# Performance work log

Hardware: AMD Instinct MI355X
Metric: run time of the kernel (lower is better)

## Reference

```python
import jax, jax.numpy as jnp
import numpy as np

B, C, L, MID, HID, OUT, K = 4096, 6, 1024, 512, 512, 256, 5
EPS = 1e-5


def _bn_eval(x, g, b, m, v):
    # BatchNorm1d eval mode on (B, C, T): normalize per channel with running stats
    inv = g / jnp.sqrt(v + EPS)
    return (x - m[None, :, None]) * inv[None, :, None] + b[None, :, None]


def setup_inputs() -> dict:
    key = jax.random.key(0)
    ks = jax.random.split(key, 12)
    s_in = 1.0 / np.sqrt(L)
    s_hid = 1.0 / np.sqrt(HID)
    inp = {
        "x": jax.random.normal(ks[0], (B, C, L), jnp.float32),
        # k stacked self-attention branches (two Linear(L, MID) each)
        "aW1": jax.random.normal(ks[1], (K, L, MID), jnp.float32) * s_in,
        "ab1": jnp.zeros((K, MID), jnp.float32),
        "aW2": jax.random.normal(ks[2], (K, L, MID), jnp.float32) * s_in,
        "ab2": jnp.zeros((K, MID), jnp.float32),
        # linearExchangeLayer: Linear(K*C, C)
        "linW": jax.random.normal(ks[3], (K * C, C), jnp.float32) / np.sqrt(K * C),
        "linb": jnp.zeros((C,), jnp.float32),
        # GraphConvolution weights
        "gW1": jax.random.normal(ks[4], (L, HID), jnp.float32) * s_in,
        "gb1": jnp.zeros((HID,), jnp.float32),
        "gW2": jax.random.normal(ks[5], (HID, OUT), jnp.float32) * s_hid,
        "gb2": jnp.zeros((OUT,), jnp.float32),
        # PReLU (single shared parameter, torch default 0.25)
        "prelu_a": jnp.array(0.25, jnp.float32),
        # BatchNorm1d params + running stats (eval mode)
        "bn1_g": jnp.ones((C,), jnp.float32),
        "bn1_b": jnp.zeros((C,), jnp.float32),
        "bn1_m": jnp.zeros((C,), jnp.float32),
        "bn1_v": jnp.ones((C,), jnp.float32),
        "bn2_g": jnp.ones((C,), jnp.float32),
        "bn2_b": jnp.zeros((C,), jnp.float32),
        "bn2_m": jnp.zeros((C,), jnp.float32),
        "bn2_v": jnp.ones((C,), jnp.float32),
    }
    return inp


def reference(x, aW1, ab1, aW2, ab2, linW, linb, gW1, gb1, gW2, gb2,
              prelu_a, bn1_g, bn1_b, bn1_m, bn1_v, bn2_g, bn2_b, bn2_m, bn2_v):
    b, c, l = x.shape
    k = aW1.shape[0]
    # --- multi-head attention adjacency: (b, c, c) ---
    q = jnp.einsum('bcl,klm->bkcm', x, aW1) + ab1[None, :, None, :]
    kv = jnp.einsum('bcl,klm->bkcm', x, aW2) + ab2[None, :, None, :]
    scores = jax.nn.softmax(jnp.einsum('bkcm,bkdm->bkcd', q, kv), axis=-1)
    # concat heads along last dim: (b, c, k*c)
    cat = scores.transpose(0, 2, 1, 3).reshape(b, c, k * c)
    A = jax.nn.softmax(cat @ linW + linb, axis=-1)  # (b, c, c)
    # --- GraphConvolution 1 (dropout identity in eval) ---
    h = jnp.einsum('bcd,bdh->bch', A, x @ gW1) + gb1
    # PReLU then BatchNorm1d
    h = jnp.where(h >= 0, h, prelu_a * h)
    h = _bn_eval(h, bn1_g, bn1_b, bn1_m, bn1_v)
    # --- GraphConvolution 2 ---
    out = jnp.einsum('bcd,bdh->bch', A, h @ gW2) + gb2
    out = _bn_eval(out, bn2_g, bn2_b, bn2_m, bn2_v)
    return out
```

## Files before the change

kernel.cpp:

```cpp
#include <hip/hip_runtime.h>
#include <hip/hip_bf16.h>


using bf16 = __hip_bfloat16;
using s16x8 = __attribute__((ext_vector_type(8))) short;
using f32x4 = __attribute__((ext_vector_type(4))) float;

#define AS1(p) ((__attribute__((address_space(1))) void*)((void*)(p)))
#define AS3(p) ((__attribute__((address_space(3))) void*)(p))

#if defined(__has_builtin)
#if __has_builtin(__builtin_amdgcn_global_load_lds)
#define HAVE_GLL 1
#endif
#endif

__device__ __forceinline__ float s2f(short s) {
  union { unsigned int u; float f; } c;
  c.u = ((unsigned int)(unsigned short)s) << 16;
  return c.f;
}
__device__ __forceinline__ short f2s(float x) {
  bf16 b = __float2bfloat16(x);
  short s;
  __builtin_memcpy(&s, &b, 2);
  return s;
}

struct GJob {
  const bf16* Bt;
  const float* bias;
  int boff;
  bf16* out;
};
struct ScJob {
  const bf16* Q;
  const bf16* KV;
  float* S;
  int head;
};

__global__ __launch_bounds__(256) void prep_kernel(
    const float* __restrict__ x, bf16* __restrict__ Xb, int do_cvt,
    const float* __restrict__ aW1, bf16* __restrict__ W1T,
    const float* __restrict__ aW2, bf16* __restrict__ W2T,
    const float* __restrict__ gW1, bf16* __restrict__ G1T,
    const float* __restrict__ gW2, bf16* __restrict__ G2T) {
  const int bid = blockIdx.x, tid = threadIdx.x;
  if (bid < 12288) {
    if (!do_cvt) return;
    int i = bid * 256 + tid;
    float4 p0 = ((const float4*)x)[i * 2];
    float4 p1 = ((const float4*)x)[i * 2 + 1];
    s16x8 v;
    v[0] = f2s(p0.x); v[1] = f2s(p0.y); v[2] = f2s(p0.z); v[3] = f2s(p0.w);
    v[4] = f2s(p1.x); v[5] = f2s(p1.y); v[6] = f2s(p1.z); v[7] = f2s(p1.w);
    ((s16x8*)Xb)[i] = v;
    return;
  }
  int r = bid - 12288;
  const float* src; short* dst; int R, C, bx, by;
  if (r < 2560) {
    int z = r >> 9, q = r & 511;
    src = aW1 + (size_t)z * 524288; dst = (short*)W1T + (size_t)z * 524288;
    R = 1024; C = 512; bx = q & 31; by = q >> 5;
  } else if (r < 5120) {
    r -= 2560;
    int z = r >> 9, q = r & 511;
    src = aW2 + (size_t)z * 524288; dst = (short*)W2T + (size_t)z * 524288;
    R = 1024; C = 512; bx = q & 31; by = q >> 5;
  } else if (r < 5632) {
    r -= 5120;
    src = gW1; dst = (short*)G1T; R = 1024; C = 512; bx = r & 31; by = r >> 5;
  } else {
    r -= 5632;
    src = gW2; dst = (short*)G2T; R = 512; C = 256; bx = r & 15; by = r >> 4;
  }
  __shared__ short tile[32][33];
  const int tx = tid & 31, ty = tid >> 5;
  const int r0 = bx * 32, c0 = by * 32;
#pragma unroll
  for (int i = 0; i < 4; ++i)
    tile[ty + i * 8][tx] = f2s(src[(size_t)(r0 + ty + i * 8) * C + c0 + tx]);
  __syncthreads();
#pragma unroll
  for (int i = 0; i < 4; ++i)
    dst[(size_t)(c0 + ty + i * 8) * R + r0 + tx] = tile[tx][ty + i * 8];
}

__device__ __forceinline__ void scores_wave(
    const bf16* __restrict__ Q, const bf16* __restrict__ KV,
    float* __restrict__ S, int head, int b0, int lane) {
  const int l16 = lane & 15, quad = lane >> 4;
  const int lr0 = (l16 < 8) ? l16 : (l16 - 8);
  const int lr = (lr0 <= 5) ? lr0 : 5;
  const int gb = (l16 < 8) ? b0 : (b0 + 1);
  const int gr = gb * 6 + lr;

  const short* qrow = (const short*)Q + (size_t)gr * 512 + quad * 8;
  const short* krow = (const short*)KV + (size_t)gr * 512 + quad * 8;

  f32x4 acc = (f32x4){0.f, 0.f, 0.f, 0.f};
#pragma unroll
  for (int kk = 0; kk < 16; ++kk) {
    s16x8 a = *(const s16x8*)(qrow + kk * 32);
    s16x8 b = *(const s16x8*)(krow + kk * 32);
    acc = __builtin_amdgcn_mfma_f32_16x16x32_bf16(a, b, acc, 0, 0, 0);
  }

  if (l16 < 6) {
#pragma unroll
    for (int r = 0; r < 4; ++r) {
      int m = quad * 4 + r;
      if (m < 6)
        S[((size_t)b0 * 5 + head) * 36 + m * 6 + l16] = acc[r];
    }
  } else if (l16 >= 8 && l16 < 14) {
#pragma unroll
    for (int r = 0; r < 4; ++r) {
      int m = quad * 4 + r;
      if (m >= 8 && m < 14)
        S[((size_t)(b0 + 1) * 5 + head) * 36 + (m - 8) * 6 + (l16 - 8)] = acc[r];
    }
  }
}

__global__ __launch_bounds__(256) void scores_mfma2(
    const bf16* __restrict__ Q0, const bf16* __restrict__ KV0,
    const bf16* __restrict__ Q1, const bf16* __restrict__ KV1,
    float* __restrict__ S, int head0) {
  const int h = blockIdx.y;
  const int lane = threadIdx.x & 63, w = threadIdx.x >> 6;
  const int b0 = (blockIdx.x * 4 + w) * 2;
  scores_wave(h ? Q1 : Q0, h ? KV1 : KV0, S, head0 + h, b0, lane);
}

template <int AF32>
__global__ __launch_bounds__(256) void gemm_bt(
    const void* __restrict__ Ag,
    const bf16* __restrict__ Bt0, const bf16* __restrict__ Bt1,
    const float* __restrict__ bias0, const float* __restrict__ bias1, int boff,
    bf16* __restrict__ out0, bf16* __restrict__ out1,
    int M, int N, int K) {
  const bf16* Bt = (blockIdx.z == 0) ? Bt0 : Bt1;
  const float* bias = (blockIdx.z == 0) ? bias0 : bias1;
  bf16* Cg = (blockIdx.z == 0) ? out0 : out1;

  __shared__ short lA[128 * 32];
  __shared__ short lB[128 * 32];

  const int tid = threadIdx.x;
  const int lane = tid & 63, w = tid >> 6;
  const int wr = w >> 1, wc = w & 1;
  const int l16 = lane & 15, quad = lane >> 4;
  const int lrow = lane >> 2;
  const int scol = (((lane & 3) ^ ((lane >> 3) & 3)) * 8);

  const size_t rm0 = (size_t)blockIdx.x * 128;
  const size_t cn0 = (size_t)blockIdx.y * 128;

  f32x4 acc[4][4];
#pragma unroll
  for (int i = 0; i < 4; ++i)
#pragma unroll
    for (int j = 0; j < 4; ++j) acc[i][j] = (f32x4){0.f, 0.f, 0.f, 0.f};

  for (int kb = 0; kb < K; kb += 32) {
#pragma unroll
    for (int t = 0; t < 2; ++t) {
      int chunk = w * 2 + t;
      int row = chunk * 16 + lrow;
      const bf16* gb = Bt + (cn0 + row) * (size_t)K + kb + scol;
#ifdef HAVE_GLL
      __builtin_amdgcn_global_load_lds(AS1(gb), AS3(lB + chunk * 512), 16, 0, 0);
#else
      *(s16x8*)(lB + chunk * 512 + lane * 8) = *(const s16x8*)gb;
#endif
      if (AF32) {
        const float* ga = (const float*)Ag + (rm0 + row) * (size_t)K + kb + scol;
        float4 p0 = *(const float4*)ga;
        float4 p1 = *(const float4*)(ga + 4);
        s16x8 v;
        v[0] = f2s(p0.x); v[1] = f2s(p0.y); v[2] = f2s(p0.z); v[3] = f2s(p0.w);
        v[4] = f2s(p1.x); v[5] = f2s(p1.y); v[6] = f2s(p1.z); v[7] = f2s(p1.w);
        *(s16x8*)(lA + chunk * 512 + lane * 8) = v;
      } else {
        const bf16* ga = (const bf16*)Ag + (rm0 + row) * (size_t)K + kb + scol;
#ifdef HAVE_GLL
        __builtin_amdgcn_global_load_lds(AS1(ga), AS3(lA + chunk * 512), 16, 0, 0);
#else
        *(s16x8*)(lA + chunk * 512 + lane * 8) = *(const s16x8*)ga;
#endif
      }
    }
    __syncthreads();

    const int q2 = (quad ^ ((l16 >> 1) & 3)) * 8;
    s16x8 af[4], bfv[4];
#pragma unroll
    for (int i = 0; i < 4; ++i) {
      af[i] = *(const s16x8*)(lA + (wr * 64 + i * 16 + l16) * 32 + q2);
      bfv[i] = *(const s16x8*)(lB + (wc * 64 + i * 16 + l16) * 32 + q2);
    }
#pragma unroll
    for (int i = 0; i < 4; ++i)
#pragma unroll
      for (int j = 0; j < 4; ++j)
        acc[i][j] = __builtin_amdgcn_mfma_f32_16x16x32_bf16(af[i], bfv[j], acc[i][j], 0, 0, 0);
    __syncthreads();
  }

#pragma unroll
  for (int j = 0; j < 4; ++j) {
    size_t col = cn0 + wc * 64 + j * 16 + l16;
    float bv = bias ? bias[boff + col] : 0.f;
#pragma unroll
    for (int i = 0; i < 4; ++i) {
      size_t rowb = rm0 + wr * 64 + i * 16 + quad * 4;
#pragma unroll
      for (int r = 0; r < 4; ++r) {
        float v = acc[i][j][r] + bv;
        Cg[(rowb + r) * (size_t)N + col] = __float2bfloat16(v);
      }
    }
  }
}

__global__ __launch_bounds__(512, 2) void gemm256_8ph(
    const bf16* __restrict__ A,
    GJob j0, GJob j1, GJob j2, GJob j3,
    int nzg, ScJob s0, ScJob s1,
    int M, int N, int K) {
  if ((int)blockIdx.z >= nzg) {
    ScJob sc = ((int)blockIdx.z == nzg) ? s0 : s1;
    const int lane = threadIdx.x & 63, w = threadIdx.x >> 6;
    const int stride = gridDim.x * gridDim.y * 8;
    const int base = ((int)blockIdx.y * gridDim.x + blockIdx.x) * 8 + w;
    for (int job = base; job < 2048; job += stride)
      scores_wave(sc.Q, sc.KV, sc.S, sc.head, job * 2, lane);
    return;
  }

  const GJob j = (blockIdx.z == 0) ? j0 : (blockIdx.z == 1) ? j1
               : (blockIdx.z == 2) ? j2 : j3;
  const bf16* Bt = j.Bt;
  const float* bias = j.bias;
  const int boff = j.boff;
  bf16* Cg = j.out;

  __shared__ __attribute__((aligned(16))) short ldsS[65536];

  const int tid = threadIdx.x;
  const int w = tid >> 6, l = tid & 63;
  const int l16 = l & 15, quad = l >> 4;
  const int wr = w >> 2, wc = w & 3;

  const size_t rm0 = (size_t)blockIdx.x * 256;
  const size_t cn0 = (size_t)blockIdx.y * 256;

  const int colS = ((l & 7) ^ (l >> 3)) * 8;
  const int rowS = w * 16 + (l >> 3);
  const short* pAs = (const short*)A + (rm0 + rowS) * (size_t)K + colS;
  const short* pBs = (const short*)Bt + (cn0 + rowS) * (size_t)K + colS;

  const int u0 = (quad ^ (l16 & 7)) * 8;
  const int u1 = ((quad + 4) ^ (l16 & 7)) * 8;

  f32x4 acc[8][4];
#pragma unroll
  for (int i = 0; i < 8; ++i)
#pragma unroll
    for (int j2i = 0; j2i < 4; ++j2i) acc[i][j2i] = (f32x4){0.f, 0.f, 0.f, 0.f};

  s16x8 af[4][2], bf0[2][2], bf1[2][2];

  const int T = K >> 6;

#ifdef HAVE_GLL
#define SA(BUF, H, KB) do {                                                          \
    __builtin_amdgcn_global_load_lds(AS1(pAs + (size_t)((H) * 128) * K + (KB)),      \
        AS3(ldsS + (BUF) * 32768 + (H) * 8192 + w * 1024), 16, 0, 0);                \
    __builtin_amdgcn_global_load_lds(AS1(pAs + (size_t)((H) * 128 + 8) * K + (KB)),  \
        AS3(ldsS + (BUF) * 32768 + (H) * 8192 + w * 1024 + 512), 16, 0, 0);          \
  } while (0)
#define SB(BUF, H, KB) do {                                                          \
    __builtin_amdgcn_global_load_lds(AS1(pBs + (size_t)((H) * 128) * K + (KB)),      \
        AS3(ldsS + (BUF) * 32768 + 16384 + (H) * 8192 + w * 1024), 16, 0, 0);        \
    __builtin_amdgcn_global_load_lds(AS1(pBs + (size_t)((H) * 128 + 8) * K + (KB)),  \
        AS3(ldsS + (BUF) * 32768 + 16384 + (H) * 8192 + w * 1024 + 512), 16, 0, 0);  \
  } while (0)
#else
#define SA(BUF, H, KB) do {                                                          \
    *(s16x8*)(ldsS + (BUF) * 32768 + (H) * 8192 + w * 1024 + l * 8) =                \
        *(const s16x8*)(pAs + (size_t)((H) * 128) * K + (KB));                       \
    *(s16x8*)(ldsS + (BUF) * 32768 + (H) * 8192 + w * 1024 + 512 + l * 8) =          \
        *(const s16x8*)(pAs + (size_t)((H) * 128 + 8) * K + (KB));                   \
  } while (0)
#define SB(BUF, H, KB) do {                                                          \
    *(s16x8*)(ldsS + (BUF) * 32768 + 16384 + (H) * 8192 + w * 1024 + l * 8) =        \
        *(const s16x8*)(pBs + (size_t)((H) * 128) * K + (KB));                       \
    *(s16x8*)(ldsS + (BUF) * 32768 + 16384 + (H) * 8192 + w * 1024 + 512 + l * 8) =  \
        *(const s16x8*)(pBs + (size_t)((H) * 128 + 8) * K + (KB));                   \
  } while (0)
#endif

#define LDA(BUF, MH) do {                                                            \
    _Pragma("unroll") for (int i = 0; i < 4; ++i) {                                  \
      const short* bse = ldsS + (BUF) * 32768 + wr * 8192 + (MH) * 4096 +            \
                         i * 1024 + l16 * 64;                                        \
      af[i][0] = *(const s16x8*)(bse + u0);                                          \
      af[i][1] = *(const s16x8*)(bse + u1);                                          \
    }                                                                                \
  } while (0)

#define LDB(BUF, NH, DST) do {                                                       \
    _Pragma("unroll") for (int n = 0; n < 2; ++n) {                                  \
      const short* bse = ldsS + (BUF) * 32768 + 16384 + (wc >> 1) * 8192 +           \
                         (wc & 1) * 4096 + (NH) * 2048 + n * 1024 + l16 * 64;        \
      DST[n][0] = *(const s16x8*)(bse + u0);                                         \
      DST[n][1] = *(const s16x8*)(bse + u1);                                         \
    }                                                                                \
  } while (0)

#define MFMAQ(MH, NH, BSET) do {                                                     \
    _Pragma("unroll") for (int i = 0; i < 4; ++i)                                    \
      _Pragma("unroll") for (int n = 0; n < 2; ++n) {                                \
        acc[(MH) * 4 + i][(NH) * 2 + n] = __builtin_amdgcn_mfma_f32_16x16x32_bf16(   \
            af[i][0], BSET[n][0], acc[(MH) * 4 + i][(NH) * 2 + n], 0, 0, 0);         \
        acc[(MH) * 4 + i][(NH) * 2 + n] = __builtin_amdgcn_mfma_f32_16x16x32_bf16(   \
            af[i][1], BSET[n][1], acc[(MH) * 4 + i][(NH) * 2 + n], 0, 0, 0);         \
      }                                                                              \
  } while (0)

#define BARX() asm volatile("s_barrier" ::: "memory")
#define LGKM0() do { asm volatile("s_waitcnt lgkmcnt(0)" ::: "memory");              \
                     __builtin_amdgcn_sched_barrier(0); } while (0)
#define VM6() do { asm volatile("s_waitcnt vmcnt(6)" ::: "memory");                  \
                   __builtin_amdgcn_sched_barrier(0); } while (0)

#define TILE_STEP(BUF, t) do {                                                       \
    const int kN_ = ((t) + 1 < T ? (t) + 1 : T - 1) << 6;                            \
    const int k2_ = ((t) + 2 < T ? (t) + 2 : T - 1) << 6;                            \
               \
    LDA(BUF, 0); LDB(BUF, 0, bf0); LDB(BUF, 1, bf1);                                 \
    SA((BUF) ^ 1, 1, kN_);                                                           \
    BARX(); LGKM0();                                                                 \
    __builtin_amdgcn_s_setprio(1); MFMAQ(0, 0, bf0); __builtin_amdgcn_s_setprio(0);  \
    BARX();                                                                          \
                        \
    SB(BUF, 0, k2_);                                                                 \
    BARX();                                                                          \
    __builtin_amdgcn_s_setprio(1); MFMAQ(0, 1, bf1); __builtin_amdgcn_s_setprio(0);  \
    BARX();                                                                          \
                                               \
    LDA(BUF, 1);                                                                     \
    SB(BUF, 1, k2_);                                                                 \
    BARX(); LGKM0();                                                                 \
    __builtin_amdgcn_s_setprio(1); MFMAQ(1, 1, bf1); __builtin_amdgcn_s_setprio(0);  \
    BARX();                                                                          \
                         \
    SA(BUF, 0, k2_);                                                                 \
    VM6();                                                                           \
    BARX();                                                                          \
    __builtin_amdgcn_s_setprio(1); MFMAQ(1, 0, bf0); __builtin_amdgcn_s_setprio(0);  \
    BARX();                                                                          \
  } while (0)

  {
    const int k1_ = (T > 1 ? 1 : 0) << 6;
    SB(0, 0, 0); SB(0, 1, 0); SA(0, 0, 0); SA(0, 1, 0);
    SB(1, 0, k1_); SB(1, 1, k1_); SA(1, 0, k1_);
    VM6();
    BARX();
  }

  for (int t = 0; t < T; t += 2) {
    TILE_STEP(0, t);
    TILE_STEP(1, t + 1);
  }

#pragma unroll
  for (int jj = 0; jj < 4; ++jj) {
    size_t col = cn0 + wc * 64 + jj * 16 + l16;
    float bv = bias ? bias[boff + col] : 0.f;
#pragma unroll
    for (int i = 0; i < 8; ++i) {
      size_t rowb = rm0 + wr * 128 + i * 16 + quad * 4;
#pragma unroll
      for (int r = 0; r < 4; ++r) {
        Cg[(rowb + r) * (size_t)N + col] = __float2bfloat16(acc[i][jj][r] + bv);
      }
    }
  }
#undef SA
#undef SB
#undef LDA
#undef LDB
#undef MFMAQ
#undef BARX
#undef LGKM0
#undef VM6
#undef TILE_STEP
}

__global__ __launch_bounds__(256) void batch_mid4(
    const float* __restrict__ S, const bf16* __restrict__ XG,
    const bf16* __restrict__ Q4, const bf16* __restrict__ KV4, int fuse5,
    const float* __restrict__ linW, const float* __restrict__ linb,
    const float* __restrict__ gb1, const float* __restrict__ prelu,
    const float* __restrict__ g1, const float* __restrict__ b1,
    const float* __restrict__ m1, const float* __restrict__ v1,
    float* __restrict__ Afull, bf16* __restrict__ H) {
  const int tid = threadIdx.x, g = tid >> 6, t = tid & 63;
  const int b = blockIdx.x * 4 + g;
  __shared__ float p[4][5][6][6];
  __shared__ float Ar[4][6][6];
  __shared__ float lw[30][6];
  __shared__ float lbv[6], sc1[6], sm1[6], sb1[6];

  if (tid < 30) {
#pragma unroll
    for (int j = 0; j < 6; ++j) lw[tid][j] = linW[tid * 6 + j];
  }
  if (tid < 6) {
    lbv[tid] = linb[tid];
    sc1[tid] = g1[tid] * rsqrtf(v1[tid] + 1e-5f);
    sm1[tid] = m1[tid];
    sb1[tid] = b1[tid];
  }
  if (fuse5 && t < 36) {
    int c = t / 6, d = t % 6;
    const s16x8* qr = (const s16x8*)((const short*)Q4 + ((size_t)b * 6 + c) * 512);
    const s16x8* kr = (const s16x8*)((const short*)KV4 + ((size_t)b * 6 + d) * 512);
    float acc = 0.f;
#pragma unroll 4
    for (int i = 0; i < 64; ++i) {
      s16x8 qa = qr[i], kb = kr[i];
#pragma unroll
      for (int j = 0; j < 8; ++j) acc += s2f(qa[j]) * s2f(kb[j]);
    }
    p[g][4][c][d] = acc;
  }
  __syncthreads();

  if (t < 30) {
    int k = t / 6, c = t % 6;
    float v[6];
    if (k == 4 && fuse5) {
#pragma unroll
      for (int d = 0; d < 6; ++d) v[d] = p[g][4][c][d];
    } else {
      const float* sp = S + ((size_t)b * 5 + k) * 36 + c * 6;
#pragma unroll
      for (int d = 0; d < 6; ++d) v[d] = sp[d];
    }
    float mx = v[0];
#pragma unroll
    for (int d = 1; d < 6; ++d) mx = fmaxf(mx, v[d]);
    float s = 0.f;
#pragma unroll
    for (int d = 0; d < 6; ++d) { v[d] = expf(v[d] - mx); s += v[d]; }
    float inv = 1.f / s;
#pragma unroll
    for (int d = 0; d < 6; ++d) p[g][k][c][d] = v[d] * inv;
  }
  __syncthreads();

  if (t < 6) {
    int c = t;
    float ap[6];
#pragma unroll
    for (int j = 0; j < 6; ++j) ap[j] = lbv[j];
    for (int k = 0; k < 5; ++k)
#pragma unroll
      for (int d = 0; d < 6; ++d) {
        float pv = p[g][k][c][d];
#pragma unroll
        for (int j = 0; j < 6; ++j) ap[j] += pv * lw[k * 6 + d][j];
      }
    float mx = ap[0];
#pragma unroll
    for (int j = 1; j < 6; ++j) mx = fmaxf(mx, ap[j]);
    float s = 0.f;
#pragma unroll
    for (int j = 0; j < 6; ++j) { ap[j] = expf(ap[j] - mx); s += ap[j]; }
    float inv = 1.f / s;
#pragma unroll
    for (int j = 0; j < 6; ++j) {
      float a = ap[j] * inv;
      Ar[g][c][j] = a;
      Afull[(size_t)b * 36 + c * 6 + j] = a;
    }
  }
  __syncthreads();

  float pa = prelu[0];
  for (int col = t; col < 512; col += 64) {
    float xg[6];
#pragma unroll
    for (int d = 0; d < 6; ++d) xg[d] = s2f(((const short*)XG)[((size_t)b * 6 + d) * 512 + col]);
    float gbv = gb1[col];
#pragma unroll
    for (int c = 0; c < 6; ++c) {
      float h = gbv;
#pragma unroll
      for (int d = 0; d < 6; ++d) h += Ar[g][c][d] * xg[d];
      h = (h >= 0.f) ? h : pa * h;
      h = (h - sm1[c]) * sc1[c] + sb1[c];
      H[((size_t)b * 6 + c) * 512 + col] = __float2bfloat16(h);
    }
  }
}

__global__ __launch_bounds__(256) void batch_out4(
    const float* __restrict__ Afull, const bf16* __restrict__ HW,
    const float* __restrict__ gb2,
    const float* __restrict__ g2, const float* __restrict__ b2,
    const float* __restrict__ m2, const float* __restrict__ v2,
    float* __restrict__ out) {
  const int tid = threadIdx.x, g = tid >> 6, t = tid & 63;
  const int b = blockIdx.x * 4 + g;
  __shared__ float Ar[4][36];
  __shared__ float sc[6], sm[6], sb[6];
  if (t < 36) Ar[g][t] = Afull[(size_t)b * 36 + t];
  if (tid < 6) {
    sc[tid] = g2[tid] * rsqrtf(v2[tid] + 1e-5f);
    sm[tid] = m2[tid];
    sb[tid] = b2[tid];
  }
  __syncthreads();
  for (int col = t; col < 256; col += 64) {
    float hw[6];
#pragma unroll
    for (int d = 0; d < 6; ++d) hw[d] = s2f(((const short*)HW)[((size_t)b * 6 + d) * 256 + col]);
    float gv = gb2[col];
#pragma unroll
    for (int c = 0; c < 6; ++c) {
      float o = gv;
#pragma unroll
      for (int d = 0; d < 6; ++d) o += Ar[g][c * 6 + d] * hw[d];
      o = (o - sm[c]) * sc[c] + sb[c];
      out[((size_t)b * 6 + c) * 256 + col] = o;
    }
  }
}

extern "C" void kernel_launch(void* const* d_in, const int* in_sizes, int n_in,
                              void* d_out, int out_size, void* d_ws, size_t ws_size,
                              hipStream_t stream) {
  const float* x    = (const float*)d_in[0];
  const float* aW1  = (const float*)d_in[1];
  const float* ab1  = (const float*)d_in[2];
  const float* aW2  = (const float*)d_in[3];
  const float* ab2  = (const float*)d_in[4];
  const float* linW = (const float*)d_in[5];
  const float* linb = (const float*)d_in[6];
  const float* gW1  = (const float*)d_in[7];
  const float* gb1  = (const float*)d_in[8];
  const float* gW2  = (const float*)d_in[9];
  const float* gb2  = (const float*)d_in[10];
  const float* prelu = (const float*)d_in[11];
  const float* bn1g = (const float*)d_in[12];
  const float* bn1b = (const float*)d_in[13];
  const float* bn1m = (const float*)d_in[14];
  const float* bn1v = (const float*)d_in[15];
  const float* bn2g = (const float*)d_in[16];
  const float* bn2b = (const float*)d_in[17];
  const float* bn2m = (const float*)d_in[18];
  const float* bn2v = (const float*)d_in[19];

  char* ws = (char*)d_ws;
  bf16* W1T   = (bf16*)(ws + 0);
  bf16* W2T   = (bf16*)(ws + 5242880);
  bf16* G1T   = (bf16*)(ws + 10485760);
  bf16* G2T   = (bf16*)(ws + 11534336);
  float* S    = (float*)(ws + 11796480);
  float* Af   = (float*)(ws + 14745600);
  bf16* BufA  = (bf16*)(ws + 15335424);
  bf16* BufB  = (bf16*)(ws + 40501248);
  bf16* Xb    = (bf16*)(ws + 65667072);
  bf16* BufA2 = (bf16*)(ws + 115998720);
  bf16* BufB2 = (bf16*)(ws + 141164544);
  bf16* BufA3 = (bf16*)(ws + 166330368);
  bf16* BufB3 = (bf16*)(ws + 191496192);
  bf16* BufA4 = (bf16*)(ws + 216662016);
  bf16* BufB4 = (bf16*)(ws + 241827840);
  const bool big  = ws_size >= 115998720ull;
  const bool big2 = ws_size >= 166330368ull;
  const bool big3 = ws_size >= 266993664ull;

  prep_kernel<<<18048, 256, 0, stream>>>(x, Xb, big ? 1 : 0,
                                         aW1, W1T, aW2, W2T, gW1, G1T, gW2, G2T);

  ScJob scz{nullptr, nullptr, nullptr, 0};

  if (big3) {
    GJob q0{W1T, ab1, 0, BufA},                 k0{W2T, ab2, 0, BufB};
    GJob q1{W1T + 524288, ab1, 512, BufA2},     k1{W2T + 524288, ab2, 512, BufB2};
    gemm256_8ph<<<dim3(96, 2, 4), 512, 0, stream>>>(
        Xb, q0, k0, q1, k1, 4, scz, scz, 24576, 512, 1024);
    GJob q2{W1T + 2 * 524288, ab1, 1024, BufA3}, k2{W2T + 2 * 524288, ab2, 1024, BufB3};
    GJob q3{W1T + 3 * 524288, ab1, 1536, BufA4}, k3{W2T + 3 * 524288, ab2, 1536, BufB4};
    ScJob sA{BufA, BufB, S, 0}, sB{BufA2, BufB2, S, 1};
    gemm256_8ph<<<dim3(96, 2, 6), 512, 0, stream>>>(
        Xb, q2, k2, q3, k3, 4, sA, sB, 24576, 512, 1024);
    GJob q4{W1T + 4 * 524288, ab1, 2048, BufA}, k4{W2T + 4 * 524288, ab2, 2048, BufB};
    GJob jxg{G1T, nullptr, 0, BufA2};
    ScJob sC{BufA3, BufB3, S, 2}, sD{BufA4, BufB4, S, 3};
    gemm256_8ph<<<dim3(96, 2, 5), 512, 0, stream>>>(
        Xb, q4, k4, jxg, jxg, 3, sC, sD, 24576, 512, 1024);
    batch_mid4<<<1024, 256, 0, stream>>>(S, BufA2, BufA, BufB, 1, linW, linb,
                                         gb1, prelu, bn1g, bn1b, bn1m, bn1v,
                                         Af, BufB2);
  } else if (big2) {
    for (int k = 0; k < 4; k += 2) {
      GJob qa{W1T + (size_t)k * 524288, ab1, k * 512, BufA};
      GJob ka{W2T + (size_t)k * 524288, ab2, k * 512, BufB};
      GJob qb{W1T + (size_t)(k + 1) * 524288, ab1, (k + 1) * 512, BufA2};
      GJob kb{W2T + (size_t)(k + 1) * 524288, ab2, (k + 1) * 512, BufB2};
      gemm256_8ph<<<dim3(96, 2, 4), 512, 0, stream>>>(
          Xb, qa, ka, qb, kb, 4, scz, scz, 24576, 512, 1024);
      scores_mfma2<<<dim3(512, 2), 256, 0, stream>>>(BufA, BufB, BufA2, BufB2, S, k);
    }
    GJob q4{W1T + 4 * 524288, ab1, 2048, BufA}, k4{W2T + 4 * 524288, ab2, 2048, BufB};
    GJob jxg{G1T, nullptr, 0, BufA2};
    gemm256_8ph<<<dim3(96, 2, 3), 512, 0, stream>>>(
        Xb, q4, k4, jxg, jxg, 4, scz, scz, 24576, 512, 1024);
    batch_mid4<<<1024, 256, 0, stream>>>(S, BufA2, BufA, BufB, 1, linW, linb,
                                         gb1, prelu, bn1g, bn1b, bn1m, bn1v,
                                         Af, BufB2);
  } else if (big) {
    for (int k = 0; k < 5; ++k) {
      GJob q{W1T + (size_t)k * 524288, ab1, k * 512, BufA};
      GJob kk{W2T + (size_t)k * 524288, ab2, k * 512, BufB};
      gemm256_8ph<<<dim3(96, 2, 2), 512, 0, stream>>>(
          Xb, q, kk, q, kk, 4, scz, scz, 24576, 512, 1024);
      scores_mfma2<<<dim3(512, 1), 256, 0, stream>>>(BufA, BufB, BufA, BufB, S, k);
    }
    GJob jxg{G1T, nullptr, 0, BufA};
    gemm256_8ph<<<dim3(96, 2, 1), 512, 0, stream>>>(
        Xb, jxg, jxg, jxg, jxg, 4, scz, scz, 24576, 512, 1024);
    batch_mid4<<<1024, 256, 0, stream>>>(S, BufA, BufA, BufA, 0, linW, linb,
                                         gb1, prelu, bn1g, bn1b, bn1m, bn1v,
                                         Af, BufB);
  } else {
    for (int k = 0; k < 5; ++k) {
      const bf16* w1 = W1T + (size_t)k * 524288;
      const bf16* w2 = W2T + (size_t)k * 524288;
      gemm_bt<1><<<dim3(192, 4, 2), 256, 0, stream>>>(
          x, w1, w2, ab1, ab2, k * 512, BufA, BufB, 24576, 512, 1024);
      scores_mfma2<<<dim3(512, 1), 256, 0, stream>>>(BufA, BufB, BufA, BufB, S, k);
    }
    gemm_bt<1><<<dim3(192, 4, 1), 256, 0, stream>>>(
        x, G1T, G1T, nullptr, nullptr, 0, BufA, BufA, 24576, 512, 1024);
    batch_mid4<<<1024, 256, 0, stream>>>(S, BufA, BufA, BufA, 0, linW, linb,
                                         gb1, prelu, bn1g, bn1b, bn1m, bn1v,
                                         Af, BufB);
  }

  bf16* Hbuf = big2 ? BufB2 : BufB;
  gemm_bt<0><<<dim3(192, 2, 1), 256, 0, stream>>>(
      Hbuf, G2T, G2T, nullptr, nullptr, 0, BufA, BufA, 24576, 256, 512);

  batch_out4<<<1024, 256, 0, stream>>>(Af, BufA, gb2, bn2g, bn2b, bn2m, bn2v,
                                       (float*)d_out);
}
```

Before: 636.6 us.

## Reassociate graph conv as (A·X)·W1, batch all projection GEMMs in one launch

Result: no change. 629.9 us (-1.1%).

```diff
diff --git a/kernel.cpp b/kernel.cpp
--- a/kernel.cpp
+++ b/kernel.cpp
@@ -33,22 +33,18 @@
   int boff;
   bf16* out;
 };
-struct ScJob {
-  const bf16* Q;
-  const bf16* KV;
-  float* S;
-  int head;
+struct GJobs10 {
+  GJob j[10];
 };
 
 __global__ __launch_bounds__(256) void prep_kernel(
-    const float* __restrict__ x, bf16* __restrict__ Xb, int do_cvt,
+    const float* __restrict__ x, bf16* __restrict__ Xb,
     const float* __restrict__ aW1, bf16* __restrict__ W1T,
     const float* __restrict__ aW2, bf16* __restrict__ W2T,
     const float* __restrict__ gW1, bf16* __restrict__ G1T,
     const float* __restrict__ gW2, bf16* __restrict__ G2T) {
   const int bid = blockIdx.x, tid = threadIdx.x;
   if (bid < 12288) {
-    if (!do_cvt) return;
     int i = bid * 256 + tid;
     float4 p0 = ((const float4*)x)[i * 2];
     float4 p1 = ((const float4*)x)[i * 2 + 1];
@@ -88,17 +84,17 @@
     dst[(size_t)(c0 + ty + i * 8) * R + r0 + tx] = tile[tx][ty + i * 8];
 }
 
-__device__ __forceinline__ void scores_wave(
-    const bf16* __restrict__ Q, const bf16* __restrict__ KV,
-    float* __restrict__ S, int head, int b0, int lane) {
+__device__ __forceinline__ void scores_grp(
+    const bf16* __restrict__ Qa, const bf16* __restrict__ Ka,
+    const bf16* __restrict__ Qb, const bf16* __restrict__ Kb,
+    int rowA, int rowB,
+    float* __restrict__ dstA, float* __restrict__ dstB,
+    int lane) {
   const int l16 = lane & 15, quad = lane >> 4;
-  const int lr0 = (l16 < 8) ? l16 : (l16 - 8);
-  const int lr = (lr0 <= 5) ? lr0 : 5;
-  const int gb = (l16 < 8) ? b0 : (b0 + 1);
-  const int gr = gb * 6 + lr;
-
-  const short* qrow = (const short*)Q + (size_t)gr * 512 + quad * 8;
-  const short* krow = (const short*)KV + (size_t)gr * 512 + quad * 8;
+  int lr = l16 & 7; if (lr > 5) lr = 5;
+  const int gr = ((l16 < 8) ? rowA : rowB) + lr;
+  const short* qrow = (const short*)((l16 < 8) ? Qa : Qb) + (size_t)gr * 512 + quad * 8;
+  const short* krow = (const short*)((l16 < 8) ? Ka : Kb) + (size_t)gr * 512 + quad * 8;
 
   f32x4 acc = (f32x4){0.f, 0.f, 0.f, 0.f};
 #pragma unroll
@@ -112,15 +108,13 @@
 #pragma unroll
     for (int r = 0; r < 4; ++r) {
       int m = quad * 4 + r;
-      if (m < 6)
-        S[((size_t)b0 * 5 + head) * 36 + m * 6 + l16] = acc[r];
+      if (m < 6) dstA[m * 6 + l16] = acc[r];
     }
   } else if (l16 >= 8 && l16 < 14) {
 #pragma unroll
     for (int r = 0; r < 4; ++r) {
       int m = quad * 4 + r;
-      if (m >= 8 && m < 14)
-        S[((size_t)(b0 + 1) * 5 + head) * 36 + (m - 8) * 6 + (l16 - 8)] = acc[r];
+      if (m >= 8 && m < 14) dstB[(m - 8) * 6 + (l16 - 8)] = acc[r];
     }
   }
 }
@@ -130,9 +124,14 @@
     const bf16* __restrict__ Q1, const bf16* __restrict__ KV1,
     float* __restrict__ S, int head0) {
   const int h = blockIdx.y;
+  const bf16* Q = h ? Q1 : Q0;
+  const bf16* KV = h ? KV1 : KV0;
+  const int head = head0 + h;
   const int lane = threadIdx.x & 63, w = threadIdx.x >> 6;
   const int b0 = (blockIdx.x * 4 + w) * 2;
-  scores_wave(h ? Q1 : Q0, h ? KV1 : KV0, S, head0 + h, b0, lane);
+  scores_grp(Q, KV, Q, KV, b0 * 6, (b0 + 1) * 6,
+             S + ((size_t)b0 * 5 + head) * 36,
+             S + ((size_t)(b0 + 1) * 5 + head) * 36, lane);
 }
 
 template <int AF32>
@@ -227,33 +226,31 @@
 }
 
 __global__ __launch_bounds__(512, 2) void gemm256_8ph(
-    const bf16* __restrict__ A,
-    GJob j0, GJob j1, GJob j2, GJob j3,
-    int nzg, ScJob s0, ScJob s1,
+    const bf16* __restrict__ A, GJobs10 jobs, int epi_z,
+    const float* __restrict__ prelu_p,
+    const float* __restrict__ bn_g, const float* __restrict__ bn_b,
+    const float* __restrict__ bn_m, const float* __restrict__ bn_v,
     int M, int N, int K) {
-  if ((int)blockIdx.z >= nzg) {
-    ScJob sc = ((int)blockIdx.z == nzg) ? s0 : s1;
-    const int lane = threadIdx.x & 63, w = threadIdx.x >> 6;
-    const int stride = gridDim.x * gridDim.y * 8;
-    const int base = ((int)blockIdx.y * gridDim.x + blockIdx.x) * 8 + w;
-    for (int job = base; job < 2048; job += stride)
-      scores_wave(sc.Q, sc.KV, sc.S, sc.head, job * 2, lane);
-    return;
-  }
-
-  const GJob j = (blockIdx.z == 0) ? j0 : (blockIdx.z == 1) ? j1
-               : (blockIdx.z == 2) ? j2 : j3;
-  const bf16* Bt = j.Bt;
-  const float* bias = j.bias;
-  const int boff = j.boff;
-  bf16* Cg = j.out;
+  const GJob jb = jobs.j[blockIdx.z];
+  const bf16* Bt = jb.Bt;
+  const float* bias = jb.bias;
+  const int boff = jb.boff;
+  bf16* Cg = jb.out;
+  const bool EPI = (epi_z == (int)blockIdx.z);
 
   __shared__ __attribute__((aligned(16))) short ldsS[65536];
+  __shared__ float epi_s[12];
 
   const int tid = threadIdx.x;
   const int w = tid >> 6, l = tid & 63;
   const int l16 = l & 15, quad = l >> 4;
   const int wr = w >> 2, wc = w & 3;
+
+  if (EPI && tid < 6) {
+    float s = bn_g[tid] * rsqrtf(bn_v[tid] + 1e-5f);
+    epi_s[tid] = s;
+    epi_s[6 + tid] = bn_b[tid] - bn_m[tid] * s;
+  }
 
   const size_t rm0 = (size_t)blockIdx.x * 256;
   const size_t cn0 = (size_t)blockIdx.y * 256;
@@ -379,18 +376,35 @@
     TILE_STEP(1, t + 1);
   }
 
+  float pa = EPI ? prelu_p[0] : 0.f;
+  short* st = ldsS + w * 8192;
 #pragma unroll
   for (int jj = 0; jj < 4; ++jj) {
-    size_t col = cn0 + wc * 64 + jj * 16 + l16;
-    float bv = bias ? bias[boff + col] : 0.f;
+    int coll = jj * 16 + l16;
+    float bv = bias ? bias[boff + (int)cn0 + wc * 64 + coll] : 0.f;
 #pragma unroll
     for (int i = 0; i < 8; ++i) {
-      size_t rowb = rm0 + wr * 128 + i * 16 + quad * 4;
 #pragma unroll
       for (int r = 0; r < 4; ++r) {
-        Cg[(rowb + r) * (size_t)N + col] = __float2bfloat16(acc[i][jj][r] + bv);
+        int rowl = i * 16 + quad * 4 + r;
+        float v = acc[i][jj][r] + bv;
+        if (EPI) {
+          v = (v >= 0.f) ? v : pa * v;
+          int c = (int)((rm0 + wr * 128 + rowl) % 6);
+          v = v * epi_s[c] + epi_s[6 + c];
+        }
+        st[rowl * 64 + coll] = f2s(v);
       }
     }
+  }
+  __syncthreads();
+#pragma unroll
+  for (int it = 0; it < 16; ++it) {
+    int rowl = it * 8 + (l >> 3);
+    int cch = (l & 7) * 8;
+    s16x8 vv = *(const s16x8*)(st + rowl * 64 + cch);
+    *(s16x8*)((short*)Cg + (rm0 + wr * 128 + rowl) * (size_t)N +
+              cn0 + wc * 64 + cch) = vv;
   }
 #undef SA
 #undef SB
@@ -403,57 +417,50 @@
 #undef TILE_STEP
 }
 
-__global__ __launch_bounds__(256) void batch_mid4(
-    const float* __restrict__ S, const bf16* __restrict__ XG,
-    const bf16* __restrict__ Q4, const bf16* __restrict__ KV4, int fuse5,
+template <int ALLP>
+__global__ __launch_bounds__(256) void mid5(
+    const float* __restrict__ S,
+    const bf16* __restrict__ Q0, const bf16* __restrict__ Q1,
+    const bf16* __restrict__ Q2, const bf16* __restrict__ Q3,
+    const bf16* __restrict__ K0, const bf16* __restrict__ K1,
+    const bf16* __restrict__ K2, const bf16* __restrict__ K3,
+    const bf16* __restrict__ Q4, const bf16* __restrict__ K4,
+    bf16* __restrict__ Xb,
     const float* __restrict__ linW, const float* __restrict__ linb,
-    const float* __restrict__ gb1, const float* __restrict__ prelu,
-    const float* __restrict__ g1, const float* __restrict__ b1,
-    const float* __restrict__ m1, const float* __restrict__ v1,
-    float* __restrict__ Afull, bf16* __restrict__ H) {
+    float* __restrict__ Afull) {
   const int tid = threadIdx.x, g = tid >> 6, t = tid & 63;
   const int b = blockIdx.x * 4 + g;
   __shared__ float p[4][5][6][6];
   __shared__ float Ar[4][6][6];
   __shared__ float lw[30][6];
-  __shared__ float lbv[6], sc1[6], sm1[6], sb1[6];
+  __shared__ float lbv[6];
 
   if (tid < 30) {
 #pragma unroll
     for (int j = 0; j < 6; ++j) lw[tid][j] = linW[tid * 6 + j];
   }
-  if (tid < 6) {
-    lbv[tid] = linb[tid];
-    sc1[tid] = g1[tid] * rsqrtf(v1[tid] + 1e-5f);
-    sm1[tid] = m1[tid];
-    sb1[tid] = b1[tid];
-  }
-  if (fuse5 && t < 36) {
-    int c = t / 6, d = t % 6;
-    const s16x8* qr = (const s16x8*)((const short*)Q4 + ((size_t)b * 6 + c) * 512);
-    const s16x8* kr = (const s16x8*)((const short*)KV4 + ((size_t)b * 6 + d) * 512);
-    float acc = 0.f;
-#pragma unroll 4
-    for (int i = 0; i < 64; ++i) {
-      s16x8 qa = qr[i], kb = kr[i];
-#pragma unroll
-      for (int j = 0; j < 8; ++j) acc += s2f(qa[j]) * s2f(kb[j]);
-    }
-    p[g][4][c][d] = acc;
+  if (tid < 6) lbv[tid] = linb[tid];
+
+  const int r6 = b * 6;
+  if (ALLP) {
+    scores_grp(Q0, K0, Q1, K1, r6, r6, &p[g][0][0][0], &p[g][1][0][0], t);
+    scores_grp(Q2, K2, Q3, K3, r6, r6, &p[g][2][0][0], &p[g][3][0][0], t);
+    scores_grp(Q4, K4, Q4, K4, r6, r6, &p[g][4][0][0], &p[g][4][0][0], t);
+  } else {
+    if (t < 36) {
+#pragma unroll
+      for (int k = 0; k < 4; ++k)
+        p[g][k][t / 6][t % 6] = S[((size_t)b * 5 + k) * 36 + t];
+    }
+    scores_grp(Q4, K4, Q4, K4, r6, r6, &p[g][4][0][0], &p[g][4][0][0], t);
   }
   __syncthreads();
 
   if (t < 30) {
     int k = t / 6, c = t % 6;
     float v[6];
-    if (k == 4 && fuse5) {
-#pragma unroll
-      for (int d = 0; d < 6; ++d) v[d] = p[g][4][c][d];
-    } else {
-      const float* sp = S + ((size_t)b * 5 + k) * 36 + c * 6;
-#pragma unroll
-      for (int d = 0; d < 6; ++d) v[d] = sp[d];
-    }
+#pragma unroll
+    for (int d = 0; d < 6; ++d) v[d] = p[g][k][c][d];
     float mx = v[0];
 #pragma unroll
     for (int d = 1; d < 6; ++d) mx = fmaxf(mx, v[d]);
@@ -494,20 +501,25 @@
   }
   __syncthreads();
 
-  float pa = prelu[0];
-  for (int col = t; col < 512; col += 64) {
-    float xg[6];
-#pragma unroll
-    for (int d = 0; d < 6; ++d) xg[d] = s2f(((const short*)XG)[((size_t)b * 6 + d) * 512 + col]);
-    float gbv = gb1[col];
+  short* xp = (short*)Xb;
+#pragma unroll
+  for (int it = 0; it < 2; ++it) {
+    int c8 = (it * 64 + t) * 8;
+    s16x8 xv[6];
+#pragma unroll
+    for (int d = 0; d < 6; ++d)
+      xv[d] = *(const s16x8*)(xp + ((size_t)r6 + d) * 1024 + c8);
 #pragma unroll
     for (int c = 0; c < 6; ++c) {
-      float h = gbv;
-#pragma unroll
-      for (int d = 0; d < 6; ++d) h += Ar[g][c][d] * xg[d];
-      h = (h >= 0.f) ? h : pa * h;
-      h = (h - sm1[c]) * sc1[c] + sb1[c];
-      H[((size_t)b * 6 + c) * 512 + col] = __float2bfloat16(h);
+      s16x8 o;
+#pragma unroll
+      for (int e = 0; e < 8; ++e) {
+        float s = 0.f;
+#pragma unroll
+        for (int d = 0; d < 6; ++d) s += Ar[g][c][d] * s2f(xv[d][e]);
+        o[e] = f2s(s);
+      }
+      *(s16x8*)(xp + ((size_t)r6 + c) * 1024 + c8) = o;
     }
   }
 }
@@ -570,98 +582,83 @@
   const float* bn2v = (const float*)d_in[19];
 
   char* ws = (char*)d_ws;
-  bf16* W1T   = (bf16*)(ws + 0);
-  bf16* W2T   = (bf16*)(ws + 5242880);
-  bf16* G1T   = (bf16*)(ws + 10485760);
-  bf16* G2T   = (bf16*)(ws + 11534336);
-  float* S    = (float*)(ws + 11796480);
-  float* Af   = (float*)(ws + 14745600);
-  bf16* BufA  = (bf16*)(ws + 15335424);
-  bf16* BufB  = (bf16*)(ws + 40501248);
-  bf16* Xb    = (bf16*)(ws + 65667072);
-  bf16* BufA2 = (bf16*)(ws + 115998720);
-  bf16* BufB2 = (bf16*)(ws + 141164544);
-  bf16* BufA3 = (bf16*)(ws + 166330368);
-  bf16* BufB3 = (bf16*)(ws + 191496192);
-  bf16* BufA4 = (bf16*)(ws + 216662016);
-  bf16* BufB4 = (bf16*)(ws + 241827840);
-  const bool big  = ws_size >= 115998720ull;
-  const bool big2 = ws_size >= 166330368ull;
-  const bool big3 = ws_size >= 266993664ull;
-
-  prep_kernel<<<18048, 256, 0, stream>>>(x, Xb, big ? 1 : 0,
-                                         aW1, W1T, aW2, W2T, gW1, G1T, gW2, G2T);
-
-  ScJob scz{nullptr, nullptr, nullptr, 0};
-
-  if (big3) {
-    GJob q0{W1T, ab1, 0, BufA},                 k0{W2T, ab2, 0, BufB};
-    GJob q1{W1T + 524288, ab1, 512, BufA2},     k1{W2T + 524288, ab2, 512, BufB2};
+  bf16* W1T = (bf16*)(ws + 0);
+  bf16* W2T = (bf16*)(ws + 5242880);
+  bf16* G1T = (bf16*)(ws + 10485760);
+  bf16* G2T = (bf16*)(ws + 11534336);
+  float* S  = (float*)(ws + 11796480);
+  float* Af = (float*)(ws + 14745600);
+  bf16* Xb  = (bf16*)(ws + 15335424);
+#define PANEL(i) ((bf16*)(ws + 65667072 + (size_t)(i) * 25165824))
+  const bool big5 = ws_size >= 292159488ull;
+
+  prep_kernel<<<18048, 256, 0, stream>>>(x, Xb, aW1, W1T, aW2, W2T, gW1, G1T, gW2, G2T);
+
+  GJobs10 J{};
+
+  if (big5) {
+    for (int h = 0; h < 4; ++h) {
+      J.j[2 * h]     = GJob{W1T + (size_t)h * 524288, ab1, h * 512, PANEL(2 * h)};
+      J.j[2 * h + 1] = GJob{W2T + (size_t)h * 524288, ab2, h * 512, PANEL(2 * h + 1)};
+    }
+    J.j[8] = GJob{W1T + 4 * 524288, ab1, 2048, (bf16*)d_out};
+    J.j[9] = GJob{W2T + 4 * 524288, ab2, 2048, PANEL(8)};
+    gemm256_8ph<<<dim3(96, 2, 10), 512, 0, stream>>>(
+        Xb, J, -1, nullptr, nullptr, nullptr, nullptr, nullptr, 24576, 512, 1024);
+
+    mid5<1><<<1024, 256, 0, stream>>>(
+        nullptr, PANEL(0), PANEL(2), PANEL(4), PANEL(6),
+        PANEL(1), PANEL(3), PANEL(5), PANEL(7),
+        (const bf16*)d_out, PANEL(8), Xb, linW, linb, Af);
+
+    GJobs10 JH{};
+    JH.j[0] = GJob{G1T, gb1, 0, PANEL(0)};
+    gemm256_8ph<<<dim3(96, 2, 1), 512, 0, stream>>>(
+        Xb, JH, 0, prelu, bn1g, bn1b, bn1m, bn1v, 24576, 512, 1024);
+
+    gemm_bt<0><<<dim3(192, 2, 1), 256, 0, stream>>>(
+        PANEL(0), G2T, G2T, nullptr, nullptr, 0, PANEL(1), PANEL(1), 24576, 256, 512);
+
+    batch_out4<<<1024, 256, 0, stream>>>(Af, PANEL(1), gb2, bn2g, bn2b, bn2m, bn2v,
+                                         (float*)d_out);
+  } else {
+    for (int h = 0; h < 2; ++h) {
+      J.j[2 * h]     = GJob{W1T + (size_t)h * 524288, ab1, h * 512, PANEL(2 * h)};
+      J.j[2 * h + 1] = GJob{W2T + (size_t)h * 524288, ab2, h * 512, PANEL(2 * h + 1)};
+    }
     gemm256_8ph<<<dim3(96, 2, 4), 512, 0, stream>>>(
-        Xb, q0, k0, q1, k1, 4, scz, scz, 24576, 512, 1024);
-    GJob q2{W1T + 2 * 524288, ab1, 1024, BufA3}, k2{W2T + 2 * 524288, ab2, 1024, BufB3};
-    GJob q3{W1T + 3 * 524288, ab1, 1536, BufA4}, k3{W2T + 3 * 524288, ab2, 1536, BufB4};
-    ScJob sA{BufA, BufB, S, 0}, sB{BufA2, BufB2, S, 1};
-    gemm256_8ph<<<dim3(96, 2, 6), 512, 0, stream>>>(
-        Xb, q2, k2, q3, k3, 4, sA, sB, 24576, 512, 1024);
-    GJob q4{W1T + 4 * 524288, ab1, 2048, BufA}, k4{W2T + 4 * 524288, ab2, 2048, BufB};
-    GJob jxg{G1T, nullptr, 0, BufA2};
-    ScJob sC{BufA3, BufB3, S, 2}, sD{BufA4, BufB4, S, 3};
-    gemm256_8ph<<<dim3(96, 2, 5), 512, 0, stream>>>(
-        Xb, q4, k4, jxg, jxg, 3, sC, sD, 24576, 512, 1024);
-    batch_mid4<<<1024, 256, 0, stream>>>(S, BufA2, BufA, BufB, 1, linW, linb,
-                                         gb1, prelu, bn1g, bn1b, bn1m, bn1v,
-                                         Af, BufB2);
-  } else if (big2) {
-    for (int k = 0; k < 4; k += 2) {
-      GJob qa{W1T + (size_t)k * 524288, ab1, k * 512, BufA};
-      GJob ka{W2T + (size_t)k * 524288, ab2, k * 512, BufB};
-      GJob qb{W1T + (size_t)(k + 1) * 524288, ab1, (k + 1) * 512, BufA2};
-      GJob kb{W2T + (size_t)(k + 1) * 524288, ab2, (k + 1) * 512, BufB2};
-      gemm256_8ph<<<dim3(96, 2, 4), 512, 0, stream>>>(
-          Xb, qa, ka, qb, kb, 4, scz, scz, 24576, 512, 1024);
-      scores_mfma2<<<dim3(512, 2), 256, 0, stream>>>(BufA, BufB, BufA2, BufB2, S, k);
-    }
-    GJob q4{W1T + 4 * 524288, ab1, 2048, BufA}, k4{W2T + 4 * 524288, ab2, 2048, BufB};
-    GJob jxg{G1T, nullptr, 0, BufA2};
-    gemm256_8ph<<<dim3(96, 2, 3), 512, 0, stream>>>(
-        Xb, q4, k4, jxg, jxg, 4, scz, scz, 24576, 512, 1024);
-    batch_mid4<<<1024, 256, 0, stream>>>(S, BufA2, BufA, BufB, 1, linW, linb,
-                                         gb1, prelu, bn1g, bn1b, bn1m, bn1v,
-                                         Af, BufB2);
-  } else if (big) {
-    for (int k = 0; k < 5; ++k) {
-      GJob q{W1T + (size_t)k * 524288, ab1, k * 512, BufA};
-      GJob kk{W2T + (size_t)k * 524288, ab2, k * 512, BufB};
-      gemm256_8ph<<<dim3(96, 2, 2), 512, 0, stream>>>(
-          Xb, q, kk, q, kk, 4, scz, scz, 24576, 512, 1024);
-      scores_mfma2<<<dim3(512, 1), 256, 0, stream>>>(BufA, BufB, BufA, BufB, S, k);
-    }
-    GJob jxg{G1T, nullptr, 0, BufA};
+        Xb, J, -1, nullptr, nullptr, nullptr, nullptr, nullptr, 24576, 512, 1024);
+    scores_mfma2<<<dim3(512, 2), 256, 0, stream>>>(
+        PANEL(0), PANEL(1), PANEL(2), PANEL(3), S, 0);
+
+    for (int h = 0; h < 2; ++h) {
+      J.j[2 * h]     = GJob{W1T + (size_t)(h + 2) * 524288, ab1, (h + 2) * 512, PANEL(4 + 2 * h)};
+      J.j[2 * h + 1] = GJob{W2T + (size_t)(h + 2) * 524288, ab2, (h + 2) * 512, PANEL(5 + 2 * h)};
+    }
+    gemm256_8ph<<<dim3(96, 2, 4), 512, 0, stream>>>(
+        Xb, J, -1, nullptr, nullptr, nullptr, nullptr, nullptr, 24576, 512, 1024);
+    scores_mfma2<<<dim3(512, 2), 256, 0, stream>>>(
+        PANEL(4), PANEL(5), PANEL(6), PANEL(7), S, 2);
+
+    J.j[0] = GJob{W1T + 4 * 524288, ab1, 2048, PANEL(0)};
+    J.j[1] = GJob{W2T + 4 * 524288, ab2, 2048, PANEL(1)};
+    gemm256_8ph<<<dim3(96, 2, 2), 512, 0, stream>>>(
+        Xb, J, -1, nullptr, nullptr, nullptr, nullptr, nullptr, 24576, 512, 1024);
+
+    mid5<0><<<1024, 256, 0, stream>>>(
+        S, nullptr, nullptr, nullptr, nullptr, nullptr, nullptr, nullptr, nullptr,
+        PANEL(0), PANEL(1), Xb, linW, linb, Af);
+
+    GJobs10 JH{};
+    JH.j[0] = GJob{G1T, gb1, 0, PANEL(2)};
     gemm256_8ph<<<dim3(96, 2, 1), 512, 0, stream>>>(
-        Xb, jxg, jxg, jxg, jxg, 4, scz, scz, 24576, 512, 1024);
-    batch_mid4<<<1024, 256, 0, stream>>>(S, BufA, BufA, BufA, 0, linW, linb,
-                                         gb1, prelu, bn1g, bn1b, bn1m, bn1v,
-                                         Af, BufB);
-  } else {
-    for (int k = 0; k < 5; ++k) {
-      const bf16* w1 = W1T + (size_t)k * 524288;
-      const bf16* w2 = W2T + (size_t)k * 524288;
-      gemm_bt<1><<<dim3(192, 4, 2), 256, 0, stream>>>(
-          x, w1, w2, ab1, ab2, k * 512, BufA, BufB, 24576, 512, 1024);
-      scores_mfma2<<<dim3(512, 1), 256, 0, stream>>>(BufA, BufB, BufA, BufB, S, k);
-    }
-    gemm_bt<1><<<dim3(192, 4, 1), 256, 0, stream>>>(
-        x, G1T, G1T, nullptr, nullptr, 0, BufA, BufA, 24576, 512, 1024);
-    batch_mid4<<<1024, 256, 0, stream>>>(S, BufA, BufA, BufA, 0, linW, linb,
-                                         gb1, prelu, bn1g, bn1b, bn1m, bn1v,
-                                         Af, BufB);
-  }
-
-  bf16* Hbuf = big2 ? BufB2 : BufB;
-  gemm_bt<0><<<dim3(192, 2, 1), 256, 0, stream>>>(
-      Hbuf, G2T, G2T, nullptr, nullptr, 0, BufA, BufA, 24576, 256, 512);
-
-  batch_out4<<<1024, 256, 0, stream>>>(Af, BufA, gb2, bn2g, bn2b, bn2m, bn2v,
-                                       (float*)d_out);
-}
+        Xb, JH, 0, prelu, bn1g, bn1b, bn1m, bn1v, 24576, 512, 1024);
+
+    gemm_bt<0><<<dim3(192, 2, 1), 256, 0, stream>>>(
+        PANEL(2), G2T, G2T, nullptr, nullptr, 0, PANEL(3), PANEL(3), 24576, 256, 512);
+
+    batch_out4<<<1024, 256, 0, stream>>>(Af, PANEL(3), gb2, bn2g, bn2b, bn2m, bn2v,
+                                         (float*)d_out);
+  }
+#undef PANEL
+}
```
